# Kernel optimization log

Hardware: AMD Instinct MI355X
Metric: run time of the kernel (lower is better)

## Reference

```python
import jax, jax.numpy as jnp
import numpy as np

B, S, D, H = 4, 2048, 1024, 16
DK = D // H


def setup_inputs() -> dict:
    key = jax.random.key(0)
    ks = jax.random.split(key, 10)
    s = 0.02  # keep linear outputs well-scaled
    causal = jnp.triu(jnp.ones((S, S), dtype=bool), k=1)  # True = masked
    return {
        "Q": jax.random.normal(ks[0], (B, S, D), dtype=jnp.float32),
        "K_V": jax.random.normal(ks[1], (B, S, D), dtype=jnp.float32),
        "mask": jnp.broadcast_to(causal, (B, S, S)),
        "Wq": jax.random.normal(ks[2], (D, D), dtype=jnp.float32) * s,
        "bq": jnp.zeros((D,), dtype=jnp.float32),
        "Wk": jax.random.normal(ks[3], (D, D), dtype=jnp.float32) * s,
        "bk": jnp.zeros((D,), dtype=jnp.float32),
        "Wv": jax.random.normal(ks[4], (D, D), dtype=jnp.float32) * s,
        "bv": jnp.zeros((D,), dtype=jnp.float32),
        "Wo": jax.random.normal(ks[5], (D, D), dtype=jnp.float32) * s,
        "bo": jnp.zeros((D,), dtype=jnp.float32),
    }


def reference(Q, K_V, mask, Wq, bq, Wk, bk, Wv, bv, Wo, bo):
    # Linear projections
    q = Q @ Wq + bq          # [B, Sq, D]
    k = K_V @ Wk + bk        # [B, Sk, D]
    v = K_V @ Wv + bv        # [B, Sk, D]
    Sq, Sk = q.shape[1], k.shape[1]
    # chunk(dim=2)+cat(dim=0) == split into H heads of size DK
    q = q.reshape(B, Sq, H, DK)
    k = k.reshape(B, Sk, H, DK)
    v = v.reshape(B, Sk, H, DK)
    scale = 1.0 / jnp.sqrt(jnp.float32(DK))
    scores = jnp.einsum("bqhd,bkhd->bhqk", q, k) * scale  # [B,H,Sq,Sk]
    # mask.repeat(head_num,1,1) == broadcast mask over heads
    scores = jnp.where(mask[:, None, :, :], -jnp.inf, scores)
    attn = jax.nn.softmax(scores, axis=-1)
    # dropout is identity in eval mode
    out = jnp.einsum("bhqk,bkhd->bqhd", attn, v).reshape(B, Sq, D)
    return out @ Wo + bo
```

## Files before the change

### kernel.cpp

```cpp
#include <hip/hip_runtime.h>

typedef unsigned short u16;
typedef __attribute__((ext_vector_type(8))) __bf16 bf16x8;
typedef __attribute__((ext_vector_type(4))) float f32x4;

#define B_  4
#define S_  2048
#define D_  1024
#define H_  16
#define DK_ 64

__device__ __forceinline__ u16 f2bf(float f) {
  unsigned u = __float_as_uint(f);
  u += 0x7fffu + ((u >> 16) & 1u);
  return (u16)(u >> 16);
}
__device__ __forceinline__ float hexp2(float f) {
  return __builtin_amdgcn_exp2f(f);
}
__device__ __forceinline__ unsigned pack_bf2(float f0, float f1) {
  return __builtin_amdgcn_perm(__float_as_uint(f1), __float_as_uint(f0), 0x07060302u);
}

__device__ __forceinline__ void load_lds16(const u16* g, u16* l) {
  __builtin_amdgcn_global_load_lds((const __attribute__((address_space(1))) void*)g,
                                   (__attribute__((address_space(3))) void*)l,
                                   16, 0, 0);
}

__global__ void cvt_bf16_2(const float* __restrict__ x0, u16* __restrict__ y0,
                           const float* __restrict__ x1, u16* __restrict__ y1, int n4) {
  int i = blockIdx.x * blockDim.x + threadIdx.x;
  const float* x = x0; u16* y = y0;
  int j = i;
  if (i >= n4) { x = x1; y = y1; j = i - n4; }
  float4 v = ((const float4*)x)[j];
  ushort4 o;
  o.x = f2bf(v.x); o.y = f2bf(v.y); o.z = f2bf(v.z); o.w = f2bf(v.w);
  ((ushort4*)y)[j] = o;
}

__global__ void transpose_cvt4(const float* __restrict__ W0, const float* __restrict__ W1,
                               const float* __restrict__ W2, const float* __restrict__ W3,
                               u16* __restrict__ T0, u16* __restrict__ T1,
                               u16* __restrict__ T2, u16* __restrict__ T3) {
  __shared__ float tile[32][33];
  const float* W = (blockIdx.z == 0) ? W0 : (blockIdx.z == 1) ? W1 : (blockIdx.z == 2) ? W2 : W3;
  u16*         T = (blockIdx.z == 0) ? T0 : (blockIdx.z == 1) ? T1 : (blockIdx.z == 2) ? T2 : T3;
  int bx = blockIdx.x * 32, by = blockIdx.y * 32;
  int tx = threadIdx.x, ty = threadIdx.y;
  #pragma unroll
  for (int i = 0; i < 32; i += 8)
    tile[ty + i][tx] = W[(size_t)(by + ty + i) * D_ + bx + tx];
  __syncthreads();
  #pragma unroll
  for (int i = 0; i < 32; i += 8)
    T[(size_t)(bx + ty + i) * D_ + by + tx] = f2bf(tile[tx][ty + i]);
}

#define GBM 128
#define GBN 256
#define GNT 16

template<int MODE>
__global__ __launch_bounds__(512, 2)
void gemm8p(const u16* __restrict__ Aq, const u16* __restrict__ Ak,
            const u16* __restrict__ Bt,
            const float* __restrict__ bq, const float* __restrict__ bk,
            const float* __restrict__ bv,
            u16* __restrict__ qp, u16* __restrict__ kp, u16* __restrict__ vpT,
            float* __restrict__ Cf, float qscale) {
  __shared__ __align__(16) u16 sm[3 * 24576];
  const int tid  = threadIdx.x;
  const int lane = tid & 63, wave = tid >> 6;
  const int bm = blockIdx.x * GBM;
  const int bn = blockIdx.y * GBN;
  const int wm = (wave >> 2) * 64, wn = (wave & 3) * 64;
  const int fm = lane & 15, fk4 = lane >> 4;
  const int K = D_;

  int path = 0;
  const u16* A = Aq;
  if constexpr (MODE == 0) { path = bn >> 10; if (path != 0) A = Ak; }

  const int sr0 = tid >> 3;
  const int kof = ((tid & 7) ^ (sr0 & 7)) * 8;
  const u16* gA = A  + (size_t)(bm + sr0) * K + kof;
  const u16* gB = Bt + (size_t)(bn + sr0) * K + kof;

#define GR(t, g) do { \
    u16* d_ = &sm[((t) % 3) * 24576 + (g) * 12288]; \
    const int ko_ = (t) * 64; \
    if ((g) == 0) { \
      load_lds16(gA + ko_,           d_ + tid * 8); \
      load_lds16(gA + 64 * K + ko_,  d_ + 4096 + tid * 8); \
      load_lds16(gB + ko_,           d_ + 8192 + tid * 8); \
    } else { \
      load_lds16(gB + 64 * K + ko_,  d_ + tid * 8); \
      load_lds16(gB + 128 * K + ko_, d_ + 4096 + tid * 8); \
      load_lds16(gB + 192 * K + ko_, d_ + 8192 + tid * 8); \
    } } while (0)

  f32x4 acc[4][4] = {};

  GR(0, 0);
  asm volatile("" ::: "memory");
  GR(0, 1);
  asm volatile("" ::: "memory");
  GR(1, 0);
  asm volatile("" ::: "memory");
  GR(1, 1);

  #pragma unroll
  for (int t = 0; t < GNT; ++t) {
    if (t < GNT - 1) asm volatile("s_waitcnt vmcnt(6)" ::: "memory");
    else             asm volatile("s_waitcnt vmcnt(0)" ::: "memory");
    __builtin_amdgcn_s_barrier();

    #pragma unroll
    for (int ks = 0; ks < 2; ++ks) {
      if (t + 2 < GNT) GR(t + 2, ks);
      asm volatile("" ::: "memory");

      const u16* rb = &sm[(t % 3) * 24576];
      const int slot = (((ks * 4) + fk4) ^ (fm & 7)) * 8;
      bf16x8 af[4], bfr[4];
      #pragma unroll
      for (int m = 0; m < 4; ++m)
        af[m] = *(const bf16x8*)&rb[(wm + m * 16 + fm) * 64 + slot];
      #pragma unroll
      for (int j = 0; j < 4; ++j)
        bfr[j] = *(const bf16x8*)&rb[(128 + wn + j * 16 + fm) * 64 + slot];
      asm volatile("s_waitcnt lgkmcnt(0)" ::: "memory");
      __builtin_amdgcn_s_setprio(1);
      #pragma unroll
      for (int m = 0; m < 4; ++m)
        #pragma unroll
        for (int j = 0; j < 4; ++j)
          acc[m][j] = __builtin_amdgcn_mfma_f32_16x16x32_bf16(af[m], bfr[j], acc[m][j], 0, 0, 0);
      __builtin_amdgcn_s_setprio(0);
    }
  }
#undef GR

  if constexpr (MODE == 0) {
    #pragma unroll
    for (int i = 0; i < 4; ++i) {
      #pragma unroll
      for (int j = 0; j < 4; ++j) {
        int colg = bn + wn + j * 16 + fm;
        int rowg0 = bm + wm + i * 16 + fk4 * 4;
        if (path == 0) {
          float bb = bq[colg];
          #pragma unroll
          for (int rg = 0; rg < 4; ++rg)
            qp[(size_t)(rowg0 + rg) * D_ + colg] = f2bf((acc[i][j][rg] + bb) * qscale);
        } else if (path == 1) {
          int ck = colg - 1024;
          float bb = bk[ck];
          #pragma unroll
          for (int rg = 0; rg < 4; ++rg)
            kp[(size_t)(rowg0 + rg) * D_ + ck] = f2bf(acc[i][j][rg] + bb);
        } else {
          int cv = colg - 2048;
          float bb = bv[cv];
          int hh = cv >> 6, dk = cv & 63;
          int bbt = rowg0 >> 11, s = rowg0 & (S_ - 1);
          ushort4 pk4;
          pk4.x = f2bf(acc[i][j][0] + bb);
          pk4.y = f2bf(acc[i][j][1] + bb);
          pk4.z = f2bf(acc[i][j][2] + bb);
          pk4.w = f2bf(acc[i][j][3] + bb);
          *(ushort4*)&vpT[(((size_t)bbt * H_ + hh) * DK_ + dk) * S_ + s] = pk4;
        }
      }
    }
  } else {
    #pragma unroll
    for (int i = 0; i < 4; ++i)
      #pragma unroll
      for (int j = 0; j < 4; ++j) {
        int colg = bn + wn + j * 16 + fm;
        float bb = bq[colg];
        #pragma unroll
        for (int rg = 0; rg < 4; ++rg) {
          int rowg = bm + wm + i * 16 + fk4 * 4 + rg;
          Cf[(size_t)rowg * D_ + colg] = acc[i][j][rg] + bb;
        }
      }
  }
}

__global__ __launch_bounds__(256, 2)
void attn_kernel(const u16* __restrict__ qp, const u16* __restrict__ kp,
                 const u16* __restrict__ vpT, u16* __restrict__ ao) {
  __shared__ u16 Ks[2][16 * 512];
  __shared__ u16 Vs[2][16 * 512];
  __shared__ u16 Ps[4 * 4 * 512];

  const int tid  = threadIdx.x;
  const int lane = tid & 63;
  const int w    = tid >> 6;
  const int fm   = lane & 15;
  const int fk4  = lane >> 4;
  const int csl  = (lane ^ ((lane >> 3) & 7)) * 8;

  const int i  = blockIdx.x;
  const int qt = 15 - (i >> 6);
  const int bh = i & 63;
  const int b  = bh >> 4;
  const int h  = bh & 15;

  const int q0 = qt * 128 + w * 32;
  const int nj = qt + 1;

  u16* Pw = &Ps[w * 2048];
  const u16* kb = kp  + (size_t)(b * S_) * D_ + h * DK_;
  const u16* vb = vpT + (size_t)((b * H_ + h) * DK_) * S_;

#define STAGEKV(bf, jj) do { \
    const int kv0_ = (jj) * 128; \
    _Pragma("unroll") \
    for (int c = 0; c < 4; ++c) { \
      int idx = 4 * w + c; \
      load_lds16(kb + (size_t)(kv0_ + (idx >> 1) * 16 + fm) * D_ + (idx & 1) * 32 + fk4 * 8, \
                 &Ks[bf][idx * 512 + lane * 8]); \
    } \
    _Pragma("unroll") \
    for (int c = 0; c < 4; ++c) { \
      int idx = 4 * w + c; \
      load_lds16(vb + (size_t)((idx & 3) * 16 + fm) * S_ + kv0_ + (idx >> 2) * 32 + fk4 * 8, \
                 &Vs[bf][idx * 512 + lane * 8]); \
    } } while (0)

  bf16x8 aq[2][2];
  #pragma unroll
  for (int qf = 0; qf < 2; ++qf)
    #pragma unroll
    for (int kh = 0; kh < 2; ++kh)
      aq[qf][kh] = *(const bf16x8*)(qp + (size_t)(b * S_ + q0 + qf * 16 + fm) * D_
                                       + h * DK_ + kh * 32 + fk4 * 8);

  f32x4 oacc[2][4] = {};
  float l0 = 0.f, l1 = 0.f;

  STAGEKV(0, 0);

  #pragma unroll 1
  for (int j = 0; j < nj; ++j) {
    const int kv0 = j * 128;
    const bool lastt = (j == qt);

    __builtin_amdgcn_s_barrier();
    if (j + 1 < nj) {
      STAGEKV((j + 1) & 1, j + 1);
      asm volatile("s_waitcnt vmcnt(8)" ::: "memory");
    } else {
      asm volatile("s_waitcnt vmcnt(0)" ::: "memory");
    }
    __builtin_amdgcn_s_barrier();

    const u16* Kb_ = &Ks[j & 1][0];
    const u16* Vb_ = &Vs[j & 1][0];

    #pragma unroll
    for (int h2 = 0; h2 < 2; ++h2) {
      #pragma unroll
      for (int mtl = 0; mtl < 4; ++mtl) {
        const int mt = h2 * 4 + mtl;
        bf16x8 kf0 = *(const bf16x8*)&Kb_[(mt * 2 + 0) * 512 + lane * 8];
        bf16x8 kf1 = *(const bf16x8*)&Kb_[(mt * 2 + 1) * 512 + lane * 8];
        f32x4 z0 = {0.f, 0.f, 0.f, 0.f}, z1 = z0;
        __builtin_amdgcn_s_setprio(1);
        z0 = __builtin_amdgcn_mfma_f32_16x16x32_bf16(kf0, aq[0][0], z0, 0, 0, 0);
        z0 = __builtin_amdgcn_mfma_f32_16x16x32_bf16(kf1, aq[0][1], z0, 0, 0, 0);
        z1 = __builtin_amdgcn_mfma_f32_16x16x32_bf16(kf0, aq[1][0], z1, 0, 0, 0);
        z1 = __builtin_amdgcn_mfma_f32_16x16x32_bf16(kf1, aq[1][1], z1, 0, 0, 0);
        __builtin_amdgcn_s_setprio(0);

        const int kvr = kv0 + mt * 16 + fk4 * 4;
        float e0[4], e1[4];
        #pragma unroll
        for (int rg = 0; rg < 4; ++rg) {
          float zz0 = z0[rg], zz1 = z1[rg];
          if (lastt) {
            if (kvr + rg > q0 + fm)      zz0 = -1e30f;
            if (kvr + rg > q0 + 16 + fm) zz1 = -1e30f;
          }
          e0[rg] = hexp2(zz0);
          e1[rg] = hexp2(zz1);
          l0 += e0[rg]; l1 += e1[rg];
        }
        const int ktl  = mtl >> 1;
        const int fk4c = (mt & 1) * 2 + (fk4 >> 1);
        const int c    = fk4c * 16 + fm;
        const int woff = (c ^ ((c >> 3) & 7)) * 8 + (fk4 & 1) * 4;
        uint2 w0, w1;
        w0.x = pack_bf2(e0[0], e0[1]); w0.y = pack_bf2(e0[2], e0[3]);
        w1.x = pack_bf2(e1[0], e1[1]); w1.y = pack_bf2(e1[2], e1[3]);
        *(uint2*)&Pw[(ktl * 2 + 0) * 512 + woff] = w0;
        *(uint2*)&Pw[(ktl * 2 + 1) * 512 + woff] = w1;
      }

      #pragma unroll
      for (int ktl = 0; ktl < 2; ++ktl) {
        const int kt = h2 * 2 + ktl;
        bf16x8 ap0 = *(const bf16x8*)&Pw[(ktl * 2 + 0) * 512 + csl];
        bf16x8 ap1 = *(const bf16x8*)&Pw[(ktl * 2 + 1) * 512 + csl];
        __builtin_amdgcn_s_setprio(1);
        #pragma unroll
        for (int nt = 0; nt < 4; ++nt) {
          bf16x8 bv = *(const bf16x8*)&Vb_[(kt * 4 + nt) * 512 + lane * 8];
          oacc[0][nt] = __builtin_amdgcn_mfma_f32_16x16x32_bf16(ap0, bv, oacc[0][nt], 0, 0, 0);
          oacc[1][nt] = __builtin_amdgcn_mfma_f32_16x16x32_bf16(ap1, bv, oacc[1][nt], 0, 0, 0);
        }
        __builtin_amdgcn_s_setprio(0);
      }
    }
  }
#undef STAGEKV

  #pragma unroll
  for (int qf = 0; qf < 2; ++qf) {
    float ls = (qf == 0) ? l0 : l1;
    ls += __shfl_xor(ls, 16, 64);
    ls += __shfl_xor(ls, 32, 64);
    #pragma unroll
    for (int rg = 0; rg < 4; ++rg) {
      float lr = __shfl(ls, fk4 * 4 + rg, 64);
      float inv = 1.0f / lr;
      int q = q0 + qf * 16 + fk4 * 4 + rg;
      #pragma unroll
      for (int nt = 0; nt < 4; ++nt) {
        float o = oacc[qf][nt][rg] * inv;
        ao[(size_t)(b * S_ + q) * D_ + h * DK_ + nt * 16 + fm] = f2bf(o);
      }
    }
  }
}

extern "C" void kernel_launch(void* const* d_in, const int* in_sizes, int n_in,
                              void* d_out, int out_size, void* d_ws, size_t ws_size,
                              hipStream_t stream) {
  const float* Q  = (const float*)d_in[0];
  const float* KV = (const float*)d_in[1];
  const float* Wq = (const float*)d_in[3];
  const float* bq = (const float*)d_in[4];
  const float* Wk = (const float*)d_in[5];
  const float* bk = (const float*)d_in[6];
  const float* Wv = (const float*)d_in[7];
  const float* bv = (const float*)d_in[8];
  const float* Wo = (const float*)d_in[9];
  const float* bo = (const float*)d_in[10];
  float* out = (float*)d_out;

  char* ws = (char*)d_ws;
  u16* Qb  = (u16*)(ws);
  u16* Kb  = (u16*)(ws + (16ull << 20));
  u16* Wqt = (u16*)(ws + (32ull << 20));
  u16* Wkt = (u16*)(ws + (34ull << 20));
  u16* Wvt = (u16*)(ws + (36ull << 20));
  u16* Wot = (u16*)(ws + (38ull << 20));
  u16* qp  = (u16*)(ws + (40ull << 20));
  u16* kp  = (u16*)(ws + (56ull << 20));
  u16* vpT = (u16*)(ws + (72ull << 20));
  u16* ao  = Qb;

  const int n4 = (B_ * S_ * D_) / 4;
  cvt_bf16_2<<<2 * n4 / 256, 256, 0, stream>>>(Q, Qb, KV, Kb, n4);

  transpose_cvt4<<<dim3(32, 32, 4), dim3(32, 8), 0, stream>>>(Wq, Wk, Wv, Wo,
                                                              Wqt, Wkt, Wvt, Wot);

  const float qscale = 0.125f * 1.44269504f;
  gemm8p<0><<<dim3(8192 / GBM, 3072 / GBN), 512, 0, stream>>>(
      Qb, Kb, Wqt, bq, bk, bv, qp, kp, vpT, nullptr, qscale);

  attn_kernel<<<1024, 256, 0, stream>>>(qp, kp, vpT, ao);

  gemm8p<1><<<dim3(8192 / GBM, 1024 / GBN), 512, 0, stream>>>(
      ao, nullptr, Wot, bo, nullptr, nullptr, nullptr, nullptr, nullptr, out, 1.0f);
}
```

Baseline: 322.2 us.

## Switch GEMM to double-buffered half-K LDS stages with per-half barriers

Replaces the three-stage 64-wide K LDS ring with two buffers, each split into two 32-wide K halves that are prefetched one half-step ahead, with a barrier before each half. This cuts LDS use per block, which may let two blocks co-reside per CU, and gives finer-grained prefetch. In exchange the XOR swizzle is dropped, the padding-free 64-byte rows may cause LDS bank conflicts, and the barrier count doubles.

```diff
diff --git a/kernel.cpp b/kernel.cpp
--- a/kernel.cpp
+++ b/kernel.cpp
@@ -70,7 +70,7 @@
             const float* __restrict__ bv,
             u16* __restrict__ qp, u16* __restrict__ kp, u16* __restrict__ vpT,
             float* __restrict__ Cf, float qscale) {
-  __shared__ __align__(16) u16 sm[3 * 24576];
+  __shared__ __align__(16) u16 sm[2 * 24576];
   const int tid  = threadIdx.x;
   const int lane = tid & 63, wave = tid >> 6;
   const int bm = blockIdx.x * GBM;
@@ -83,23 +83,20 @@
   const u16* A = Aq;
   if constexpr (MODE == 0) { path = bn >> 10; if (path != 0) A = Ak; }
 
-  const int sr0 = tid >> 3;
-  const int kof = ((tid & 7) ^ (sr0 & 7)) * 8;
-  const u16* gA = A  + (size_t)(bm + sr0) * K + kof;
-  const u16* gB = Bt + (size_t)(bn + sr0) * K + kof;
-
-#define GR(t, g) do { \
-    u16* d_ = &sm[((t) % 3) * 24576 + (g) * 12288]; \
-    const int ko_ = (t) * 64; \
-    if ((g) == 0) { \
-      load_lds16(gA + ko_,           d_ + tid * 8); \
-      load_lds16(gA + 64 * K + ko_,  d_ + 4096 + tid * 8); \
-      load_lds16(gB + ko_,           d_ + 8192 + tid * 8); \
-    } else { \
-      load_lds16(gB + 64 * K + ko_,  d_ + tid * 8); \
-      load_lds16(gB + 128 * K + ko_, d_ + 4096 + tid * 8); \
-      load_lds16(gB + 192 * K + ko_, d_ + 8192 + tid * 8); \
-    } } while (0)
+  const int sr  = tid >> 2;
+  const int sl  = tid & 3;
+  const int kof = sl * 8;
+  const u16* gA  = A  + (size_t)(bm + sr) * K + kof;
+  const u16* gB0 = Bt + (size_t)(bn + sr) * K + kof;
+  const u16* gB1 = Bt + (size_t)(bn + 128 + sr) * K + kof;
+
+#define GR(t, ks) do { \
+    u16* lr_ = &sm[((t) & 1) * 24576 + (ks) * 12288]; \
+    const int ko_ = (t) * 64 + (ks) * 32; \
+    load_lds16(gA  + ko_, lr_ + tid * 8); \
+    load_lds16(gB0 + ko_, lr_ + 4096 + tid * 8); \
+    load_lds16(gB1 + ko_, lr_ + 8192 + tid * 8); \
+  } while (0)
 
   f32x4 acc[4][4] = {};
 
@@ -108,30 +105,27 @@
   GR(0, 1);
   asm volatile("" ::: "memory");
   GR(1, 0);
-  asm volatile("" ::: "memory");
-  GR(1, 1);
 
   #pragma unroll
   for (int t = 0; t < GNT; ++t) {
-    if (t < GNT - 1) asm volatile("s_waitcnt vmcnt(6)" ::: "memory");
-    else             asm volatile("s_waitcnt vmcnt(0)" ::: "memory");
-    __builtin_amdgcn_s_barrier();
-
     #pragma unroll
     for (int ks = 0; ks < 2; ++ks) {
-      if (t + 2 < GNT) GR(t + 2, ks);
+      if (t < GNT - 1)  asm volatile("s_waitcnt vmcnt(6)" ::: "memory");
+      else if (ks == 0) asm volatile("s_waitcnt vmcnt(3)" ::: "memory");
+      else              asm volatile("s_waitcnt vmcnt(0)" ::: "memory");
+      __builtin_amdgcn_s_barrier();
+      if (ks == 0) { if (t + 1 < GNT) GR(t + 1, 1); }
+      else         { if (t + 2 < GNT) GR(t + 2, 0); }
       asm volatile("" ::: "memory");
 
-      const u16* rb = &sm[(t % 3) * 24576];
-      const int slot = (((ks * 4) + fk4) ^ (fm & 7)) * 8;
+      const u16* rb = &sm[(t & 1) * 24576 + ks * 12288];
       bf16x8 af[4], bfr[4];
       #pragma unroll
       for (int m = 0; m < 4; ++m)
-        af[m] = *(const bf16x8*)&rb[(wm + m * 16 + fm) * 64 + slot];
+        af[m] = *(const bf16x8*)&rb[(wm + m * 16 + fm) * 32 + fk4 * 8];
       #pragma unroll
       for (int j = 0; j < 4; ++j)
-        bfr[j] = *(const bf16x8*)&rb[(128 + wn + j * 16 + fm) * 64 + slot];
-      asm volatile("s_waitcnt lgkmcnt(0)" ::: "memory");
+        bfr[j] = *(const bf16x8*)&rb[(128 + wn + j * 16 + fm) * 32 + fk4 * 8];
       __builtin_amdgcn_s_setprio(1);
       #pragma unroll
       for (int m = 0; m < 4; ++m)
```

Result: no change. 321.9 us (-0.1%).
